# Kernel tuning notes

Hardware: AMD Instinct MI355X
Metric: run time of the kernel (lower is better)

Reference implementation:

```python
import jax, jax.numpy as jnp
import numpy as np

N_NODES = 100000
N_EDGES = 1600000
FEAT_DIM = 64
IN_DIM = FEAT_DIM + 3  # feat + xyz


def setup_inputs() -> dict:
    key = jax.random.key(0)
    k1, k2, k3, k4, k5 = jax.random.split(key, 5)
    xyz = jax.random.normal(k1, (N_NODES, 3), dtype=jnp.float32)
    feat = jax.random.normal(k2, (N_NODES, FEAT_DIM), dtype=jnp.float32)
    edge_index = jax.random.randint(k3, (2, N_EDGES), 0, N_NODES, dtype=jnp.int64)
    # MLP params (Linear stored as [in, out] for x @ W + b)
    W1 = jax.random.normal(k4, (2 * IN_DIM, FEAT_DIM), dtype=jnp.float32) * (1.0 / np.sqrt(2 * IN_DIM))
    b1 = jnp.zeros((FEAT_DIM,), dtype=jnp.float32)
    W2 = jax.random.normal(k5, (FEAT_DIM, FEAT_DIM), dtype=jnp.float32) * (1.0 / np.sqrt(FEAT_DIM))
    b2 = jnp.zeros((FEAT_DIM,), dtype=jnp.float32)
    return {"xyz": xyz, "feat": feat, "edge_index": edge_index,
            "W1": W1, "b1": b1, "W2": W2, "b2": b2}


def reference(xyz, feat, edge_index, W1, b1, W2, b2):
    # node features: cat([feat, xyz]) -> [N, C+3]
    x = jnp.concatenate([feat, xyz], axis=-1)
    src = edge_index[0]  # j (source / neighbor)
    dst = edge_index[1]  # i (target, aggregation index)
    x_i = x[dst]                       # [E, C+3]
    x_j = x[src]                       # [E, C+3]
    # EdgeConv message: mlp(cat([x_i, x_j - x_i]))
    m = jnp.concatenate([x_i, x_j - x_i], axis=-1)   # [E, 2*(C+3)]
    h = jax.nn.relu(m @ W1 + b1) @ W2 + b2           # [E, C]
    n = x.shape[0]
    agg = jax.ops.segment_max(h, dst, num_segments=n)  # [N, C]
    # nodes with no incoming edges get 0 (matches PyG scatter-max fill)
    deg = jax.ops.segment_sum(jnp.ones((dst.shape[0],), h.dtype), dst, num_segments=n)
    return jnp.where(deg[:, None] > 0, agg, jnp.zeros_like(agg))
```

## Files before the change

kernel.cpp:

```cpp
#include <hip/hip_runtime.h>
#include <stdint.h>

#define N_NODES 100000
#define FEAT 64
#define NB 64
#define SC_CHUNK 8192
#define NBKT 1563
#define BKT_CAP 1400
#define BIAS 512.0f

typedef __attribute__((ext_vector_type(8))) _Float16 half8;
typedef __attribute__((ext_vector_type(2))) _Float16 half2v;
typedef __attribute__((ext_vector_type(2))) __fp16 fp16x2;
typedef __attribute__((ext_vector_type(4))) float f32x4;

__device__ __forceinline__ uint32_t enc_key(float f) {
    uint32_t u = __float_as_uint(f);
    return (u & 0x80000000u) ? ~u : (u | 0x80000000u);
}
__device__ __forceinline__ float dec_key(uint32_t k) {
    return __uint_as_float((k & 0x80000000u) ? (k & 0x7FFFFFFFu) : ~k);
}
__device__ __forceinline__ uint32_t pk_f16(float a, float b) {
    union { fp16x2 h; uint32_t u; } cv;
    cv.h = __builtin_amdgcn_cvt_pkrtz(a, b);
    return cv.u;
}

#define W2T_OFF 0
#define AMB_OFF 4096
#define BM_OFF  8384
#define W2P_OFF 12672
#define U_OFF   16384
#define V_OFF   (U_OFF + N_NODES * FEAT / 2)
#define GCNT_OFF (U_OFF + N_NODES * FEAT)
#define SRT_OFF  (GCNT_OFF + 2048)

__global__ __launch_bounds__(256) void transform_kernel(
    const float* __restrict__ W1, const float* __restrict__ W2,
    float* __restrict__ ws, int full)
{
    int i = blockIdx.x * 256 + threadIdx.x;
    if (full && i < 2048)
        ((uint32_t*)ws)[GCNT_OFF + i] = 0u;
    if (i < 4096) {
        int c2 = i >> 6, c = i & 63;
        ws[W2T_OFF + i] = W2[c * 64 + c2];
    } else if (full && i < 8384) {
        int j = i - 4096;
        ws[AMB_OFF + j] = W1[j] - W1[j + 67 * 64];
    } else if (full && i < 12672) {
        int j = i - 8384;
        ws[BM_OFF + j] = W1[j + 67 * 64];
    } else if (full && i < 16768) {
        int p = i - 12672;
        int j = p & 7, c2lo = (p >> 3) & 15, quad = (p >> 7) & 3;
        int h = (p >> 9) & 1, n4 = (p >> 10) & 3;
        int k = h * 32 + quad * 8 + j;
        int n = n4 * 16 + c2lo;
        ((_Float16*)(ws + W2P_OFF))[p] = (_Float16)W2[k * 64 + n];
    }
}

__global__ __launch_bounds__(256) void node_kernel(
    const float* __restrict__ xyz, const float* __restrict__ feat,
    const float* __restrict__ b1, const float* __restrict__ ws,
    uint16_t* __restrict__ U, uint16_t* __restrict__ V, int nN)
{
    int n = blockIdx.x * 256 + threadIdx.x;
    int half = blockIdx.y;
    if (n >= nN) return;
    const float* __restrict__ W = ws + (half ? BM_OFF : AMB_OFF);

    float acc[FEAT];
    if (half == 0) {
        #pragma unroll
        for (int c = 0; c < FEAT; ++c) acc[c] = b1[c];
    } else {
        #pragma unroll
        for (int c = 0; c < FEAT; ++c) acc[c] = 0.0f;
    }

    const float* f = feat + (size_t)n * FEAT;
    #pragma unroll 1
    for (int k = 0; k < 64; k += 4) {
        float4 x4 = *(const float4*)(f + k);
        float xv[4] = {x4.x, x4.y, x4.z, x4.w};
        #pragma unroll
        for (int q = 0; q < 4; ++q) {
            const float* __restrict__ w = W + (k + q) * 64;
            #pragma unroll
            for (int c = 0; c < FEAT; ++c)
                acc[c] = fmaf(xv[q], w[c], acc[c]);
        }
    }
    const float* p = xyz + (size_t)n * 3;
    #pragma unroll
    for (int k3 = 0; k3 < 3; ++k3) {
        float xv = p[k3];
        const float* __restrict__ w = W + (64 + k3) * 64;
        #pragma unroll
        for (int c = 0; c < FEAT; ++c)
            acc[c] = fmaf(xv, w[c], acc[c]);
    }
    uint32_t* outp = (uint32_t*)((half ? V : U) + (size_t)n * FEAT);
    #pragma unroll
    for (int c = 0; c < 32; ++c)
        outp[c] = pk_f16(acc[2*c], acc[2*c+1]);
}

__global__ __launch_bounds__(256) void bucket_kernel(
    const int* __restrict__ ei, uint32_t* __restrict__ gcnt,
    uint32_t* __restrict__ sorted, int nE)
{
    __shared__ uint32_t svals[SC_CHUNK];
    __shared__ uint16_t sbkt[SC_CHUNK];
    __shared__ uint32_t hist[NBKT];
    __shared__ uint32_t base[NBKT + 1];
    __shared__ uint32_t segs[256];

    int t = threadIdx.x;
    int e0 = blockIdx.x * SC_CHUNK;
    int cnt = min(SC_CHUNK, nE - e0);

    for (int i = t; i < NBKT; i += 256) hist[i] = 0;
    __syncthreads();
    for (int i = t; i < cnt; i += 256) {
        int dst = ei[nE + e0 + i];
        atomicAdd(&hist[dst >> 6], 1u);
    }
    __syncthreads();
    {
        const int SEG = 7;
        int lo = t * SEG, hi = min(lo + SEG, NBKT);
        uint32_t s = 0;
        for (int i = lo; i < hi; ++i) s += hist[i];
        segs[t] = s;
        __syncthreads();
        for (int d = 1; d < 256; d <<= 1) {
            uint32_t x = (t >= d) ? segs[t - d] : 0;
            __syncthreads();
            segs[t] += x;
            __syncthreads();
        }
        uint32_t run = (t == 0) ? 0 : segs[t - 1];
        for (int i = lo; i < hi; ++i) { uint32_t c = hist[i]; base[i] = run; run += c; }
        if (t == 255) base[NBKT] = run;
    }
    __syncthreads();
    for (int i = t; i < NBKT; i += 256) hist[i] = base[i];
    __syncthreads();
    for (int i = t; i < cnt; i += 256) {
        int src = ei[e0 + i];
        int dst = ei[nE + e0 + i];
        int b = dst >> 6;
        uint32_t pos = atomicAdd(&hist[b], 1u);
        svals[pos] = (uint32_t)src | ((uint32_t)(dst & 63) << 20);
        sbkt[pos] = (uint16_t)b;
    }
    __syncthreads();
    for (int b = t; b < NBKT; b += 256) {
        uint32_t c = base[b + 1] - base[b];
        hist[b] = c ? atomicAdd(&gcnt[b], c) : 0u;
    }
    __syncthreads();
    for (int i = t; i < cnt; i += 256) {
        uint32_t b = sbkt[i];
        uint32_t off = hist[b] + ((uint32_t)i - base[b]);
        if (off < BKT_CAP)
            sorted[(size_t)b * BKT_CAP + off] = svals[i];
    }
}

#define LOADE(G, DSV, VV0, VV1, UU0, UU1) do {                               \
        int e_c_ = min((G) + el, cnt - 1);                                   \
        uint32_t val_ = ssrt[e_c_];                                          \
        DSV = *(const uint4*)(ssrt + (G) + quad * 4);                        \
        int src_ = (int)(val_ & 0xFFFFFu);                                   \
        const uint32_t* vr_ = (const uint32_t*)(V + (size_t)src_ * FEAT);    \
        VV0 = *(const uint4*)(vr_ + quad * 4);                               \
        VV1 = *(const uint4*)(vr_ + 16 + quad * 4);                          \
        const uint32_t* ur_ = ushare + (int)(val_ >> 20) * 32;               \
        UU0 = *(const uint4*)(ur_ + quad * 4);                               \
        UU1 = *(const uint4*)(ur_ + 16 + quad * 4);                          \
    } while (0)

__global__ __launch_bounds__(256) void agg_kernel(
    const uint32_t* __restrict__ gcnt, const uint32_t* __restrict__ sorted,
    const uint16_t* __restrict__ U, const uint16_t* __restrict__ V,
    const float* __restrict__ ws_w2p, const float* __restrict__ b2,
    float* __restrict__ out, int nN)
{
    __shared__ int      lmax[NB * 65];
    __shared__ uint32_t ushare[NB * 32];
    __shared__ uint32_t ssrt[BKT_CAP + 16];
    __shared__ uint32_t shist[NB];

    int bkt = blockIdx.x;
    int nb0 = bkt * NB;
    int rows = min(NB, nN - nb0);
    int cnt = min((int)gcnt[bkt], BKT_CAP);
    int t = threadIdx.x;

    for (int i = t; i < NB * 65; i += 256) lmax[i] = 0;
    if (t < NB) shist[t] = 0;
    {
        const uint32_t* usrc = (const uint32_t*)(U + (size_t)nb0 * FEAT);
        for (int i = t; i < rows * 32; i += 256) ushare[i] = usrc[i];
    }
    const uint32_t* bsrc = sorted + (size_t)bkt * BKT_CAP;
    __syncthreads();
    for (int i = t; i < cnt; i += 256)
        atomicAdd(&shist[bsrc[i] >> 20], 1u);
    __syncthreads();
    if (t < NB) {
        uint32_t v = shist[t];
        uint32_t run = v;
        #pragma unroll
        for (int d = 1; d < 64; d <<= 1) {
            uint32_t x = (uint32_t)__shfl_up((int)run, (unsigned)d, 64);
            if (t >= d) run += x;
        }
        shist[t] = run - v;
    }
    __syncthreads();
    for (int i = t; i < cnt; i += 256) {
        uint32_t v = bsrc[i];
        uint32_t pos = atomicAdd(&shist[v >> 20], 1u);
        ssrt[pos] = v;
    }
    __syncthreads();

    int lane = t & 63;
    int wave = t >> 6;
    int el = lane & 15, quad = lane >> 4;

    const uint4* w2p = (const uint4*)ws_w2p;
    union { uint4 u4; half8 h8; } bfr[8];
    #pragma unroll
    for (int q8 = 0; q8 < 8; ++q8)
        bfr[q8].u4 = w2p[(q8 * 4 + quad) * 16 + el];
    float b2v[4];
    #pragma unroll
    for (int n4 = 0; n4 < 4; ++n4) b2v[n4] = b2[n4 * 16 + el] + BIAS;

    const half2v zero2 = {(_Float16)0.0f, (_Float16)0.0f};

    uint4 dsv_c, vv_c0, vv_c1, uu_c0, uu_c1;
    int g = wave * 16;
    if (g < cnt) LOADE(g, dsv_c, vv_c0, vv_c1, uu_c0, uu_c1);

    #pragma unroll 1
    for (; g < cnt; g += 64) {
        int gn = g + 64;
        int gl = (gn < cnt) ? gn : g;
        uint4 dsv_n, vv_n0, vv_n1, uu_n0, uu_n1;
        LOADE(gl, dsv_n, vv_n0, vv_n1, uu_n0, uu_n1);

        union { uint4 u4; half8 h8; } afr[2];
        #pragma unroll
        for (int h = 0; h < 2; ++h) {
            uint4 uu = h ? uu_c1 : uu_c0;
            uint4 vv = h ? vv_c1 : vv_c0;
            uint32_t ua[4] = {uu.x, uu.y, uu.z, uu.w};
            uint32_t va[4] = {vv.x, vv.y, vv.z, vv.w};
            uint32_t pk[4];
            #pragma unroll
            for (int p = 0; p < 4; ++p) {
                union { uint32_t u; half2v h2; } cu, cv2, ct;
                cu.u = ua[p]; cv2.u = va[p];
                ct.h2 = __builtin_elementwise_max(cu.h2 + cv2.h2, zero2);
                pk[p] = ct.u;
            }
            afr[h].u4 = make_uint4(pk[0], pk[1], pk[2], pk[3]);
        }

        f32x4 acc[4];
        #pragma unroll
        for (int n4 = 0; n4 < 4; ++n4)
            acc[n4] = (f32x4){b2v[n4], b2v[n4], b2v[n4], b2v[n4]};
        #pragma unroll
        for (int n4 = 0; n4 < 4; ++n4) {
            acc[n4] = __builtin_amdgcn_mfma_f32_16x16x32_f16(afr[0].h8, bfr[n4*2+0].h8, acc[n4], 0, 0, 0);
            acc[n4] = __builtin_amdgcn_mfma_f32_16x16x32_f16(afr[1].h8, bfr[n4*2+1].h8, acc[n4], 0, 0, 0);
        }

        int d0 = (int)(dsv_c.x >> 20), d1 = (int)(dsv_c.y >> 20);
        int d2 = (int)(dsv_c.z >> 20), d3 = (int)(dsv_c.w >> 20);
        int eb = g + quad * 4;
        bool ok0 = eb < cnt, ok1 = eb + 1 < cnt;
        bool ok2 = eb + 2 < cnt, ok3 = eb + 3 < cnt;
        bool m0 = (d0 == d1) & ok1;
        bool m1 = (d1 == d2) & ok2;
        bool m2 = (d2 == d3) & ok3;
        #pragma unroll
        for (int n4 = 0; n4 < 4; ++n4) {
            if (m0) acc[n4][1] = fmaxf(acc[n4][1], acc[n4][0]);
            if (m1) acc[n4][2] = fmaxf(acc[n4][2], acc[n4][1]);
            if (m2) acc[n4][3] = fmaxf(acc[n4][3], acc[n4][2]);
        }
        if (ok0 & !m0) {
            #pragma unroll
            for (int n4 = 0; n4 < 4; ++n4)
                atomicMax(&lmax[d0 * 65 + n4 * 16 + el], __float_as_int(acc[n4][0]));
        }
        if (ok1 & !m1) {
            #pragma unroll
            for (int n4 = 0; n4 < 4; ++n4)
                atomicMax(&lmax[d1 * 65 + n4 * 16 + el], __float_as_int(acc[n4][1]));
        }
        if (ok2 & !m2) {
            #pragma unroll
            for (int n4 = 0; n4 < 4; ++n4)
                atomicMax(&lmax[d2 * 65 + n4 * 16 + el], __float_as_int(acc[n4][2]));
        }
        if (ok3) {
            #pragma unroll
            for (int n4 = 0; n4 < 4; ++n4)
                atomicMax(&lmax[d3 * 65 + n4 * 16 + el], __float_as_int(acc[n4][3]));
        }

        dsv_c = dsv_n;
        vv_c0 = vv_n0; vv_c1 = vv_n1;
        uu_c0 = uu_n0; uu_c1 = uu_n1;
    }
    __syncthreads();

    for (int i = t; i < rows * FEAT; i += 256) {
        int r = i >> 6, c = i & 63;
        int k = lmax[r * 65 + c];
        out[(size_t)(nb0 + r) * FEAT + c] = k ? (__int_as_float(k) - BIAS) : 0.0f;
    }
}
#undef LOADE

__device__ __forceinline__ void rank1_update(
    float* __restrict__ h, float xi, float d,
    const float* __restrict__ A, const float* __restrict__ B)
{
    #pragma unroll
    for (int c = 0; c < FEAT; ++c)
        h[c] = fmaf(xi, A[c], fmaf(d, B[c], h[c]));
}

__global__ __launch_bounds__(256) void edge_fused_kernel(
    const float* __restrict__ xyz, const float* __restrict__ feat,
    const int* __restrict__ ei,
    const float* __restrict__ W1, const float* __restrict__ b1,
    const float* __restrict__ ws, const float* __restrict__ b2,
    uint32_t* __restrict__ keys, int nE)
{
    int e = blockIdx.x * 256 + threadIdx.x;
    if (e >= nE) return;
    int src = ei[e];
    int dst = ei[nE + e];
    const float* __restrict__ W2T = ws + W2T_OFF;

    float h[FEAT];
    #pragma unroll
    for (int c = 0; c < FEAT; ++c) h[c] = b1[c];

    const float* fi = feat + (size_t)dst * FEAT;
    const float* fj = feat + (size_t)src * FEAT;
    #pragma unroll 1
    for (int k = 0; k < 64; k += 4) {
        float4 a = *(const float4*)(fi + k);
        float4 b = *(const float4*)(fj + k);
        rank1_update(h, a.x, b.x - a.x, W1 + (k + 0) * 64, W1 + (67 + k + 0) * 64);
        rank1_update(h, a.y, b.y - a.y, W1 + (k + 1) * 64, W1 + (67 + k + 1) * 64);
        rank1_update(h, a.z, b.z - a.z, W1 + (k + 2) * 64, W1 + (67 + k + 2) * 64);
        rank1_update(h, a.w, b.w - a.w, W1 + (k + 3) * 64, W1 + (67 + k + 3) * 64);
    }
    {
        const float* pi = xyz + (size_t)dst * 3;
        const float* pj = xyz + (size_t)src * 3;
        #pragma unroll
        for (int k3 = 0; k3 < 3; ++k3) {
            float xi = pi[k3];
            rank1_update(h, xi, pj[k3] - xi, W1 + (64 + k3) * 64, W1 + (131 + k3) * 64);
        }
    }
    #pragma unroll
    for (int c = 0; c < FEAT; ++c) h[c] = fmaxf(h[c], 0.0f);

    uint32_t* krow = keys + (size_t)dst * FEAT;
    #pragma unroll 1
    for (int c2 = 0; c2 < FEAT; c2 += 4) {
        float o0 = b2[c2 + 0], o1 = b2[c2 + 1];
        float o2 = b2[c2 + 2], o3 = b2[c2 + 3];
        const float* w0 = W2T + (c2 + 0) * 64;
        const float* w1 = W2T + (c2 + 1) * 64;
        const float* w2 = W2T + (c2 + 2) * 64;
        const float* w3 = W2T + (c2 + 3) * 64;
        #pragma unroll
        for (int c = 0; c < FEAT; ++c) {
            float hv = h[c];
            o0 = fmaf(hv, w0[c], o0);
            o1 = fmaf(hv, w1[c], o1);
            o2 = fmaf(hv, w2[c], o2);
            o3 = fmaf(hv, w3[c], o3);
        }
        uint32_t k0 = enc_key(o0), k1 = enc_key(o1);
        uint32_t k2 = enc_key(o2), k3 = enc_key(o3);
        uint4 cur = *(const uint4*)(krow + c2);
        if (k0 > cur.x) atomicMax(&krow[c2 + 0], k0);
        if (k1 > cur.y) atomicMax(&krow[c2 + 1], k1);
        if (k2 > cur.z) atomicMax(&krow[c2 + 2], k2);
        if (k3 > cur.w) atomicMax(&krow[c2 + 3], k3);
    }
}

__global__ __launch_bounds__(256) void decode_kernel(
    uint32_t* __restrict__ keys, int n4)
{
    int i = blockIdx.x * 256 + threadIdx.x;
    if (i >= n4) return;
    uint4 k = ((const uint4*)keys)[i];
    float4 r;
    r.x = k.x ? dec_key(k.x) : 0.0f;
    r.y = k.y ? dec_key(k.y) : 0.0f;
    r.z = k.z ? dec_key(k.z) : 0.0f;
    r.w = k.w ? dec_key(k.w) : 0.0f;
    ((float4*)keys)[i] = r;
}

extern "C" void kernel_launch(void* const* d_in, const int* in_sizes, int n_in,
                              void* d_out, int out_size, void* d_ws, size_t ws_size,
                              hipStream_t stream)
{
    const float* xyz  = (const float*)d_in[0];
    const float* feat = (const float*)d_in[1];
    const int*   ei   = (const int*)d_in[2];
    const float* W1   = (const float*)d_in[3];
    const float* b1   = (const float*)d_in[4];
    const float* W2   = (const float*)d_in[5];
    const float* b2   = (const float*)d_in[6];

    int nE = in_sizes[2] / 2;
    float* ws = (float*)d_ws;

    size_t need_words = (size_t)SRT_OFF + (size_t)NBKT * BKT_CAP;
    int full = (ws_size >= need_words * 4) ? 1 : 0;

    transform_kernel<<<66, 256, 0, stream>>>(W1, W2, ws, full);

    if (full) {
        uint16_t* U = (uint16_t*)(ws + U_OFF);
        uint16_t* V = (uint16_t*)(ws + V_OFF);
        uint32_t* gcnt   = (uint32_t*)(ws + GCNT_OFF);
        uint32_t* sorted = (uint32_t*)(ws + SRT_OFF);

        dim3 ngrid((N_NODES + 255) / 256, 2);
        node_kernel<<<ngrid, 256, 0, stream>>>(xyz, feat, b1, ws, U, V, N_NODES);
        bucket_kernel<<<(nE + SC_CHUNK - 1) / SC_CHUNK, 256, 0, stream>>>(
            ei, gcnt, sorted, nE);
        agg_kernel<<<NBKT, 256, 0, stream>>>(
            gcnt, sorted, U, V, ws + W2P_OFF, b2, (float*)d_out, N_NODES);
    } else {
        uint32_t* keys = (uint32_t*)d_out;
        hipMemsetAsync(d_out, 0, (size_t)out_size * sizeof(float), stream);
        edge_fused_kernel<<<(nE + 255) / 256, 256, 0, stream>>>(
            xyz, feat, ei, W1, b1, ws, b2, keys, nE);
        decode_kernel<<<(out_size / 4 + 255) / 256, 256, 0, stream>>>(
            keys, out_size / 4);
    }
}
```

Before: 203.9 us.

## Merge node transform and edge bucketing into one launch, vectorize memory ops

Merges the node-projection kernel and the edge-bucketing kernel into a single launch: the first blocks bucket edges and the remaining blocks compute the U/V node projections, so the two independent stages can run at the same time and one launch is saved. It also vectorizes the edge-index loads, the scatter loop, the U/V fp16 stores, the ushare fill and the output writes to 128-bit accesses. In agg_kernel, bucket entries are kept in registers between the histogram and the scatter pass instead of being reloaded from global memory. The merged kernel carries the bucketing blocks' large shared-memory footprint for every block, which may lower occupancy for the node-projection blocks. The register cache (RVN 6) covers up to 1536 entries, which exceeds BKT_CAP, so no entries are dropped.

Result: faster. 175.0 us (-14.2%).

```diff
diff --git a/kernel.cpp b/kernel.cpp
--- a/kernel.cpp
+++ b/kernel.cpp
@@ -7,6 +7,7 @@
 #define SC_CHUNK 8192
 #define NBKT 1563
 #define BKT_CAP 1400
+#define RVN 6
 #define BIAS 512.0f
 
 typedef __attribute__((ext_vector_type(8))) _Float16 half8;
@@ -62,13 +63,110 @@
     }
 }
 
-__global__ __launch_bounds__(256) void node_kernel(
+__global__ __launch_bounds__(256) void nodebkt_kernel(
     const float* __restrict__ xyz, const float* __restrict__ feat,
     const float* __restrict__ b1, const float* __restrict__ ws,
-    uint16_t* __restrict__ U, uint16_t* __restrict__ V, int nN)
-{
-    int n = blockIdx.x * 256 + threadIdx.x;
-    int half = blockIdx.y;
+    uint16_t* __restrict__ U, uint16_t* __restrict__ V, int nN,
+    const int* __restrict__ ei, uint32_t* __restrict__ gcnt,
+    uint32_t* __restrict__ sorted, int nE, int nBkt)
+{
+    __shared__ uint32_t svals[SC_CHUNK];
+    __shared__ uint16_t sbkt[SC_CHUNK];
+    __shared__ uint32_t hist[NBKT];
+    __shared__ uint32_t base[NBKT + 1];
+    __shared__ uint32_t segs[256];
+
+    int t = threadIdx.x;
+
+    if ((int)blockIdx.x < nBkt) {
+        int e0 = blockIdx.x * SC_CHUNK;
+        int cnt = min(SC_CHUNK, nE - e0);
+        int cnt4 = cnt & ~3;
+
+        for (int i = t; i < NBKT; i += 256) hist[i] = 0;
+        __syncthreads();
+        for (int i = t * 4; i < cnt4; i += 1024) {
+            uint4 d4 = *(const uint4*)(ei + nE + e0 + i);
+            atomicAdd(&hist[d4.x >> 6], 1u);
+            atomicAdd(&hist[d4.y >> 6], 1u);
+            atomicAdd(&hist[d4.z >> 6], 1u);
+            atomicAdd(&hist[d4.w >> 6], 1u);
+        }
+        for (int i = cnt4 + t; i < cnt; i += 256)
+            atomicAdd(&hist[ei[nE + e0 + i] >> 6], 1u);
+        __syncthreads();
+        {
+            const int SEG = 7;
+            int lo = t * SEG, hi = min(lo + SEG, NBKT);
+            uint32_t s = 0;
+            for (int i = lo; i < hi; ++i) s += hist[i];
+            segs[t] = s;
+            __syncthreads();
+            for (int d = 1; d < 256; d <<= 1) {
+                uint32_t x = (t >= d) ? segs[t - d] : 0;
+                __syncthreads();
+                segs[t] += x;
+                __syncthreads();
+            }
+            uint32_t run = (t == 0) ? 0 : segs[t - 1];
+            for (int i = lo; i < hi; ++i) { uint32_t c = hist[i]; base[i] = run; run += c; }
+            if (t == 255) base[NBKT] = run;
+        }
+        __syncthreads();
+        for (int i = t; i < NBKT; i += 256) hist[i] = base[i];
+        __syncthreads();
+        for (int i = t * 4; i < cnt4; i += 1024) {
+            uint4 s4 = *(const uint4*)(ei + e0 + i);
+            uint4 d4 = *(const uint4*)(ei + nE + e0 + i);
+            uint32_t sa[4] = {(uint32_t)s4.x, (uint32_t)s4.y, (uint32_t)s4.z, (uint32_t)s4.w};
+            uint32_t da[4] = {(uint32_t)d4.x, (uint32_t)d4.y, (uint32_t)d4.z, (uint32_t)d4.w};
+            #pragma unroll
+            for (int k = 0; k < 4; ++k) {
+                uint32_t b = da[k] >> 6;
+                uint32_t pos = atomicAdd(&hist[b], 1u);
+                svals[pos] = sa[k] | ((da[k] & 63u) << 20);
+                sbkt[pos] = (uint16_t)b;
+            }
+        }
+        for (int i = cnt4 + t; i < cnt; i += 256) {
+            uint32_t src = (uint32_t)ei[e0 + i];
+            uint32_t dst = (uint32_t)ei[nE + e0 + i];
+            uint32_t b = dst >> 6;
+            uint32_t pos = atomicAdd(&hist[b], 1u);
+            svals[pos] = src | ((dst & 63u) << 20);
+            sbkt[pos] = (uint16_t)b;
+        }
+        __syncthreads();
+        for (int b = t; b < NBKT; b += 256) {
+            uint32_t c = base[b + 1] - base[b];
+            hist[b] = c ? atomicAdd(&gcnt[b], c) : 0u;
+        }
+        __syncthreads();
+        for (int i = t * 4; i < cnt4; i += 1024) {
+            ushort4 b4 = *(const ushort4*)(sbkt + i);
+            uint4 v4 = *(const uint4*)(svals + i);
+            uint32_t ba[4] = {b4.x, b4.y, b4.z, b4.w};
+            uint32_t va[4] = {v4.x, v4.y, v4.z, v4.w};
+            #pragma unroll
+            for (int k = 0; k < 4; ++k) {
+                uint32_t b = ba[k];
+                uint32_t off = hist[b] + ((uint32_t)(i + k) - base[b]);
+                if (off < BKT_CAP)
+                    sorted[(size_t)b * BKT_CAP + off] = va[k];
+            }
+        }
+        for (int i = cnt4 + t; i < cnt; i += 256) {
+            uint32_t b = sbkt[i];
+            uint32_t off = hist[b] + ((uint32_t)i - base[b]);
+            if (off < BKT_CAP)
+                sorted[(size_t)b * BKT_CAP + off] = svals[i];
+        }
+        return;
+    }
+
+    int nb = blockIdx.x - nBkt;
+    int half = nb & 1;
+    int n = (nb >> 1) * 256 + t;
     if (n >= nN) return;
     const float* __restrict__ W = ws + (half ? BM_OFF : AMB_OFF);
 
@@ -103,72 +201,15 @@
         for (int c = 0; c < FEAT; ++c)
             acc[c] = fmaf(xv, w[c], acc[c]);
     }
-    uint32_t* outp = (uint32_t*)((half ? V : U) + (size_t)n * FEAT);
-    #pragma unroll
-    for (int c = 0; c < 32; ++c)
-        outp[c] = pk_f16(acc[2*c], acc[2*c+1]);
-}
-
-__global__ __launch_bounds__(256) void bucket_kernel(
-    const int* __restrict__ ei, uint32_t* __restrict__ gcnt,
-    uint32_t* __restrict__ sorted, int nE)
-{
-    __shared__ uint32_t svals[SC_CHUNK];
-    __shared__ uint16_t sbkt[SC_CHUNK];
-    __shared__ uint32_t hist[NBKT];
-    __shared__ uint32_t base[NBKT + 1];
-    __shared__ uint32_t segs[256];
-
-    int t = threadIdx.x;
-    int e0 = blockIdx.x * SC_CHUNK;
-    int cnt = min(SC_CHUNK, nE - e0);
-
-    for (int i = t; i < NBKT; i += 256) hist[i] = 0;
-    __syncthreads();
-    for (int i = t; i < cnt; i += 256) {
-        int dst = ei[nE + e0 + i];
-        atomicAdd(&hist[dst >> 6], 1u);
-    }
-    __syncthreads();
-    {
-        const int SEG = 7;
-        int lo = t * SEG, hi = min(lo + SEG, NBKT);
-        uint32_t s = 0;
-        for (int i = lo; i < hi; ++i) s += hist[i];
-        segs[t] = s;
-        __syncthreads();
-        for (int d = 1; d < 256; d <<= 1) {
-            uint32_t x = (t >= d) ? segs[t - d] : 0;
-            __syncthreads();
-            segs[t] += x;
-            __syncthreads();
-        }
-        uint32_t run = (t == 0) ? 0 : segs[t - 1];
-        for (int i = lo; i < hi; ++i) { uint32_t c = hist[i]; base[i] = run; run += c; }
-        if (t == 255) base[NBKT] = run;
-    }
-    __syncthreads();
-    for (int i = t; i < NBKT; i += 256) hist[i] = base[i];
-    __syncthreads();
-    for (int i = t; i < cnt; i += 256) {
-        int src = ei[e0 + i];
-        int dst = ei[nE + e0 + i];
-        int b = dst >> 6;
-        uint32_t pos = atomicAdd(&hist[b], 1u);
-        svals[pos] = (uint32_t)src | ((uint32_t)(dst & 63) << 20);
-        sbkt[pos] = (uint16_t)b;
-    }
-    __syncthreads();
-    for (int b = t; b < NBKT; b += 256) {
-        uint32_t c = base[b + 1] - base[b];
-        hist[b] = c ? atomicAdd(&gcnt[b], c) : 0u;
-    }
-    __syncthreads();
-    for (int i = t; i < cnt; i += 256) {
-        uint32_t b = sbkt[i];
-        uint32_t off = hist[b] + ((uint32_t)i - base[b]);
-        if (off < BKT_CAP)
-            sorted[(size_t)b * BKT_CAP + off] = svals[i];
+    uint4* outp = (uint4*)((half ? V : U) + (size_t)n * FEAT);
+    #pragma unroll
+    for (int q = 0; q < 8; ++q) {
+        uint4 o;
+        o.x = pk_f16(acc[8*q + 0], acc[8*q + 1]);
+        o.y = pk_f16(acc[8*q + 2], acc[8*q + 3]);
+        o.z = pk_f16(acc[8*q + 4], acc[8*q + 5]);
+        o.w = pk_f16(acc[8*q + 6], acc[8*q + 7]);
+        outp[q] = o;
     }
 }
 
@@ -205,13 +246,22 @@
     for (int i = t; i < NB * 65; i += 256) lmax[i] = 0;
     if (t < NB) shist[t] = 0;
     {
-        const uint32_t* usrc = (const uint32_t*)(U + (size_t)nb0 * FEAT);
-        for (int i = t; i < rows * 32; i += 256) ushare[i] = usrc[i];
+        const uint4* usrc4 = (const uint4*)(U + (size_t)nb0 * FEAT);
+        for (int i = t; i < rows * 8; i += 256) ((uint4*)ushare)[i] = usrc4[i];
     }
     const uint32_t* bsrc = sorted + (size_t)bkt * BKT_CAP;
     __syncthreads();
-    for (int i = t; i < cnt; i += 256)
-        atomicAdd(&shist[bsrc[i] >> 20], 1u);
+
+    uint32_t rv[RVN];
+    #pragma unroll
+    for (int j = 0; j < RVN; ++j) {
+        int i = t + j * 256;
+        if (i < cnt) {
+            uint32_t v = bsrc[i];
+            rv[j] = v;
+            atomicAdd(&shist[v >> 20], 1u);
+        }
+    }
     __syncthreads();
     if (t < NB) {
         uint32_t v = shist[t];
@@ -224,10 +274,14 @@
         shist[t] = run - v;
     }
     __syncthreads();
-    for (int i = t; i < cnt; i += 256) {
-        uint32_t v = bsrc[i];
-        uint32_t pos = atomicAdd(&shist[v >> 20], 1u);
-        ssrt[pos] = v;
+    #pragma unroll
+    for (int j = 0; j < RVN; ++j) {
+        int i = t + j * 256;
+        if (i < cnt) {
+            uint32_t v = rv[j];
+            uint32_t pos = atomicAdd(&shist[v >> 20], 1u);
+            ssrt[pos] = v;
+        }
     }
     __syncthreads();
 
@@ -326,10 +380,17 @@
     }
     __syncthreads();
 
-    for (int i = t; i < rows * FEAT; i += 256) {
+    for (int i = t * 4; i < rows * FEAT; i += 1024) {
         int r = i >> 6, c = i & 63;
-        int k = lmax[r * 65 + c];
-        out[(size_t)(nb0 + r) * FEAT + c] = k ? (__int_as_float(k) - BIAS) : 0.0f;
+        int lb = r * 65 + c;
+        int k0 = lmax[lb + 0], k1 = lmax[lb + 1];
+        int k2 = lmax[lb + 2], k3 = lmax[lb + 3];
+        float4 o;
+        o.x = k0 ? (__int_as_float(k0) - BIAS) : 0.0f;
+        o.y = k1 ? (__int_as_float(k1) - BIAS) : 0.0f;
+        o.z = k2 ? (__int_as_float(k2) - BIAS) : 0.0f;
+        o.w = k3 ? (__int_as_float(k3) - BIAS) : 0.0f;
+        *(float4*)(out + (size_t)(nb0 + r) * FEAT + c) = o;
     }
 }
 #undef LOADE
@@ -450,10 +511,10 @@
         uint32_t* gcnt   = (uint32_t*)(ws + GCNT_OFF);
         uint32_t* sorted = (uint32_t*)(ws + SRT_OFF);
 
-        dim3 ngrid((N_NODES + 255) / 256, 2);
-        node_kernel<<<ngrid, 256, 0, stream>>>(xyz, feat, b1, ws, U, V, N_NODES);
-        bucket_kernel<<<(nE + SC_CHUNK - 1) / SC_CHUNK, 256, 0, stream>>>(
-            ei, gcnt, sorted, nE);
+        int nBkt = (nE + SC_CHUNK - 1) / SC_CHUNK;
+        int nodeBlocks = ((N_NODES + 255) / 256) * 2;
+        nodebkt_kernel<<<nBkt + nodeBlocks, 256, 0, stream>>>(
+            xyz, feat, b1, ws, U, V, N_NODES, ei, gcnt, sorted, nE, nBkt);
         agg_kernel<<<NBKT, 256, 0, stream>>>(
             gcnt, sorted, U, V, ws + W2P_OFF, b2, (float*)d_out, N_NODES);
     } else {
```
